# Kernel tuning notes

Hardware: AMD Instinct MI355X
Metric: run time of the kernel (lower is better)

Reference implementation:

```python
import jax, jax.numpy as jnp
import numpy as np

B, D, M, R, C = 4096, 16, 4, 2048, 10
EPS = 1e-9


def setup_inputs() -> dict:
    key = jax.random.key(0)
    k1, k2, k3, k4, k5 = jax.random.split(key, 5)
    x = jax.random.normal(k1, (B, D), dtype=jnp.float32)
    centers = jax.random.normal(k2, (D, M), dtype=jnp.float32)
    widths = jax.random.uniform(k3, (D, M), dtype=jnp.float32, minval=0.5, maxval=1.5)
    consequents = jax.random.uniform(k4, (R, D + 1, C), dtype=jnp.float32)
    rules = jax.random.randint(k5, (R, D), 0, M, dtype=jnp.int32)
    return {"x": x, "centers": centers, "widths": widths,
            "consequents": consequents, "rules": rules}


def reference(x, centers, widths, consequents, rules):
    batch = x.shape[0]
    # Gaussian membership values: (B, D, M)
    mfs = jnp.exp(-((x[:, :, None] - centers[None]) ** 2) / (2.0 * widths[None] ** 2))
    # Gather per-rule memberships: rule_mfs[b, d, r] = mfs[b, d, rules[r, d]] -> (B, D, R)
    idx = jnp.broadcast_to(rules.T[None].astype(jnp.int32), (batch, rules.shape[1], rules.shape[0]))
    rule_mfs = jnp.take_along_axis(mfs, idx, axis=2)
    # Firing strengths: product over input dims -> (B, R)
    fs = jnp.prod(rule_mfs, axis=1)
    norm_fs = fs / (jnp.sum(fs, axis=1, keepdims=True) + EPS)
    # Extended input with bias column -> (B, D+1)
    x_ext = jnp.concatenate([x, jnp.ones((batch, 1), dtype=x.dtype)], axis=1)
    # Faithful to torch.einsum('bi,rjc->brc', ...): i and j are both summed out
    rule_vals = jnp.einsum('bi,rjc->brc', x_ext, consequents)  # (B, R, C)
    out = jnp.einsum('br,brc->bc', norm_fs, rule_vals)  # (B, C)
    return out, norm_fs, x_ext
```

## Files before the change

kernel.cpp:

```cpp
#include <hip/hip_runtime.h>

#define BB 4096
#define DD 16
#define MM 4
#define RR 2048
#define CC 10
#define TB 4
#define RPT (RR / 256)

typedef __attribute__((ext_vector_type(4))) float f32x4;
typedef __attribute__((ext_vector_type(2))) float f32x2;
typedef __attribute__((ext_vector_type(4))) unsigned short u16x4;

__device__ __forceinline__ unsigned short f2bf(float x) {
    union { float f; unsigned u; } v; v.f = x;
    unsigned b = v.u + 0x7FFFu + ((v.u >> 16) & 1u);
    return (unsigned short)(b >> 16);
}
__device__ __forceinline__ float bf2f(unsigned short h) {
    union { unsigned u; float f; } v; v.u = ((unsigned)h) << 16;
    return v.f;
}

__global__ __launch_bounds__(256) void prep_kernel(
    const float* __restrict__ cons, const int* __restrict__ rules,
    float* __restrict__ wsum4a, float* __restrict__ wsum4b,
    float* __restrict__ wsum2, unsigned int* __restrict__ codes)
{
    int gid = blockIdx.x * 256 + threadIdx.x;
    if (gid < RR * CC) {
        int r = gid / CC, c = gid - r * CC;
        const float* cr = cons + (size_t)r * (DD + 1) * CC + c;
        float s = 0.0f;
#pragma unroll
        for (int j = 0; j < DD + 1; ++j) s += cr[j * CC];
        if (c < 4)      wsum4a[r * 4 + c] = s;
        else if (c < 8) wsum4b[r * 4 + (c - 4)] = s;
        else            wsum2[r * 2 + (c - 8)] = s;
    }
    if (gid < RR) {
        const int* rrp = rules + gid * DD;
        unsigned int code = 0;
#pragma unroll
        for (int g = 0; g < 4; ++g) {
            unsigned int byt = 0;
#pragma unroll
            for (int k = 0; k < 4; ++k)
                byt |= (((unsigned int)rrp[g * 4 + k]) & 3u) << (2 * k);
            code |= byt << (8 * g);
        }
        codes[gid] = code;
    }
}

__global__ __launch_bounds__(256, 4) void anfis_main(
    const float* __restrict__ x, const float* __restrict__ centers,
    const float* __restrict__ widths, const f32x4* __restrict__ wsum4a,
    const f32x4* __restrict__ wsum4b, const f32x2* __restrict__ wsum2,
    const unsigned int* __restrict__ codes,
    float* __restrict__ out, float* __restrict__ norm_fs, float* __restrict__ x_ext)
{
    __shared__ __align__(16) char pool[4 * 256 * sizeof(f32x4)];
    f32x4 (*QUAD4)[256] = (f32x4 (*)[256])pool;
    float (*RED)[68]    = (float (*)[68])pool;

    __shared__ u16x4 FS[RR];
    __shared__ float MF[TB][64];
    __shared__ f32x4 PAIR4[8][16];
    __shared__ float xs[TB][DD];
    __shared__ float sx[TB];
    __shared__ float wpart[4][TB];
    __shared__ float invl[TB];
    __shared__ float oscale[TB];
    __shared__ float part2[TB * CC][4];

    const int tid = threadIdx.x;
    const int b0 = blockIdx.x * TB;
    const int lane = tid & 63;
    const int wv = tid >> 6;

    if (tid < TB * (DD + 1)) {
        int row = tid / (DD + 1), col = tid % (DD + 1);
        float v = (col < DD) ? x[(b0 + row) * DD + col] : 1.0f;
        if (col < DD) xs[row][col] = v;
        x_ext[(b0 + row) * (DD + 1) + col] = v;
    }
    __syncthreads();
    if (tid < TB) {
        float s = 1.0f;
#pragma unroll
        for (int d = 0; d < DD; ++d) s += xs[tid][d];
        sx[tid] = s;
    }

    {
        int row = tid >> 6, dm = tid & 63, d = dm >> 2, m = dm & 3;
        float c = centers[d * MM + m];
        float w = widths[d * MM + m];
        float z = xs[row][d] - c;
        MF[row][dm] = expf(-(z * z) / (2.0f * w * w));
    }
    __syncthreads();

    if (tid < 8 * 16) {
        int p = tid >> 4, e = tid & 15;
        int i0 = e & 3, i1 = e >> 2;
        f32x4 v;
#pragma unroll
        for (int row = 0; row < TB; ++row)
            v[row] = MF[row][(2 * p) * 4 + i0] * MF[row][(2 * p + 1) * 4 + i1];
        PAIR4[p][e] = v;
    }
    __syncthreads();

#pragma unroll
    for (int i = tid; i < 4 * 256; i += 256) {
        int g = i >> 8, e = i & 255;
        QUAD4[g][e] = PAIR4[2 * g][e & 15] * PAIR4[2 * g + 1][e >> 4];
    }
    __syncthreads();

    float acc[TB][CC];
#pragma unroll
    for (int row = 0; row < TB; ++row)
#pragma unroll
        for (int c = 0; c < CC; ++c) acc[row][c] = 0.0f;

    f32x4 svec = {0.0f, 0.0f, 0.0f, 0.0f};

#pragma unroll 1
    for (int j = 0; j < RPT; ++j) {
        int r = tid + 256 * j;
        unsigned int code = codes[r];
        f32x4 q0 = QUAD4[0][code & 255u];
        f32x4 q1 = QUAD4[1][(code >> 8) & 255u];
        f32x4 q2 = QUAD4[2][(code >> 16) & 255u];
        f32x4 q3 = QUAD4[3][code >> 24];
        f32x4 p = (q0 * q1) * (q2 * q3);
        svec += p;

        u16x4 fh;
        fh.x = f2bf(p[0]); fh.y = f2bf(p[1]);
        fh.z = f2bf(p[2]); fh.w = f2bf(p[3]);
        FS[r] = fh;

        const f32x4 wa = wsum4a[r];
        const f32x4 wb = wsum4b[r];
        const f32x2 wcp = wsum2[r];
        const float wc[CC] = {wa.x, wa.y, wa.z, wa.w, wb.x,
                              wb.y, wb.z, wb.w, wcp.x, wcp.y};
#pragma unroll
        for (int row = 0; row < TB; ++row)
#pragma unroll
            for (int c = 0; c < CC; ++c)
                acc[row][c] = fmaf(p[row], wc[c], acc[row][c]);
    }

#pragma unroll
    for (int row = 0; row < TB; ++row) {
        float s = svec[row];
#pragma unroll
        for (int off = 32; off > 0; off >>= 1) s += __shfl_xor(s, off, 64);
        if (lane == 0) wpart[wv][row] = s;
    }
    __syncthreads();
    if (tid < TB) {
        float t = wpart[0][tid] + wpart[1][tid] + wpart[2][tid] + wpart[3][tid];
        float inv = 1.0f / (t + 1e-9f);
        invl[tid] = inv;
        oscale[tid] = sx[tid] * inv;
    }
    __syncthreads();

    const float inv0 = invl[0], inv1 = invl[1], inv2 = invl[2], inv3 = invl[3];

#pragma unroll 1
    for (int j = 0; j < RPT; ++j) {
        int r = tid + 256 * j;
        u16x4 fh = FS[r];
        norm_fs[(size_t)(b0 + 0) * RR + r] = bf2f(fh.x) * inv0;
        norm_fs[(size_t)(b0 + 1) * RR + r] = bf2f(fh.y) * inv1;
        norm_fs[(size_t)(b0 + 2) * RR + r] = bf2f(fh.z) * inv2;
        norm_fs[(size_t)(b0 + 3) * RR + r] = bf2f(fh.w) * inv3;
    }

#pragma unroll
    for (int row = 0; row < TB; ++row) {
#pragma unroll
        for (int c = 0; c < CC; ++c) {
            float s = acc[row][c];
            s += __shfl_xor(s, 1, 64);
            s += __shfl_xor(s, 2, 64);
            if ((lane & 3) == 0) RED[row * CC + c][wv * 16 + (lane >> 2)] = s;
        }
    }
    __syncthreads();
    if (tid < 160) {
        int v = tid % 40, ch = tid / 40;
        float s = 0.0f;
        int base = ch * 16;
#pragma unroll
        for (int i = 0; i < 16; ++i) s += RED[v][base + i];
        part2[v][ch] = s;
    }
    __syncthreads();
    if (tid < TB * CC) {
        float val = part2[tid][0] + part2[tid][1] + part2[tid][2] + part2[tid][3];
        int row = tid / CC, c = tid % CC;
        out[(b0 + row) * CC + c] = oscale[row] * val;
    }
}

extern "C" void kernel_launch(void* const* d_in, const int* in_sizes, int n_in,
                              void* d_out, int out_size, void* d_ws, size_t ws_size,
                              hipStream_t stream) {
    const float* x       = (const float*)d_in[0];
    const float* centers = (const float*)d_in[1];
    const float* widths  = (const float*)d_in[2];
    const float* cons    = (const float*)d_in[3];
    const int*   rules   = (const int*)d_in[4];

    float* out_p     = (float*)d_out;
    float* norm_fs_p = out_p + (size_t)BB * CC;
    float* x_ext_p   = norm_fs_p + (size_t)BB * RR;

    float* wsum4a = (float*)d_ws;
    float* wsum4b = wsum4a + (size_t)RR * 4;
    float* wsum2  = wsum4b + (size_t)RR * 4;
    unsigned int* codes = (unsigned int*)(wsum2 + (size_t)RR * 2);

    prep_kernel<<<(RR * CC + 255) / 256, 256, 0, stream>>>(cons, rules, wsum4a,
                                                           wsum4b, wsum2, codes);
    anfis_main<<<BB / TB, 256, 0, stream>>>(x, centers, widths,
                                            (const f32x4*)wsum4a,
                                            (const f32x4*)wsum4b,
                                            (const f32x2*)wsum2, codes,
                                            out_p, norm_fs_p, x_ext_p);
}
```

Measured before the change: 86.74 us.

## Split main kernel into reduction pass and recompute-and-store pass

The fused kernel is split in two. The first kernel computes the firing-strength sums, the per-row inverse normaliser (written to workspace) and the output. The second kernel rebuilds the membership tables, recomputes the firing strengths and writes norm_fs directly. This removes the 16KB bf16 shared buffer and its rounding, which lowers shared memory per block and may raise occupancy. In exchange the table build and product work run twice and there is an extra launch.

```diff
diff --git a/kernel.cpp b/kernel.cpp
--- a/kernel.cpp
+++ b/kernel.cpp
@@ -10,17 +10,6 @@
 
 typedef __attribute__((ext_vector_type(4))) float f32x4;
 typedef __attribute__((ext_vector_type(2))) float f32x2;
-typedef __attribute__((ext_vector_type(4))) unsigned short u16x4;
-
-__device__ __forceinline__ unsigned short f2bf(float x) {
-    union { float f; unsigned u; } v; v.f = x;
-    unsigned b = v.u + 0x7FFFu + ((v.u >> 16) & 1u);
-    return (unsigned short)(b >> 16);
-}
-__device__ __forceinline__ float bf2f(unsigned short h) {
-    union { unsigned u; float f; } v; v.u = ((unsigned)h) << 16;
-    return v.f;
-}
 
 __global__ __launch_bounds__(256) void prep_kernel(
     const float* __restrict__ cons, const int* __restrict__ rules,
@@ -53,24 +42,47 @@
     }
 }
 
-__global__ __launch_bounds__(256, 4) void anfis_main(
+#define BUILD_TABLES(QUADP)  do { \
+    { int row = tid >> 6, dm = tid & 63, d = dm >> 2, m = dm & 3; \
+      float c = centers[d * MM + m]; \
+      float w = widths[d * MM + m]; \
+      float z = xs[row][d] - c; \
+      MF[row][dm] = expf(-(z * z) / (2.0f * w * w)); } \
+    __syncthreads(); \
+    if (tid < 8 * 16) { \
+        int p = tid >> 4, e = tid & 15; \
+        int i0 = e & 3, i1 = e >> 2; \
+        f32x4 v; \
+        _Pragma("unroll") \
+        for (int row = 0; row < TB; ++row) \
+            v[row] = MF[row][(2 * p) * 4 + i0] * MF[row][(2 * p + 1) * 4 + i1]; \
+        PAIR4[p][e] = v; \
+    } \
+    __syncthreads(); \
+    _Pragma("unroll") \
+    for (int i = tid; i < 4 * 256; i += 256) { \
+        int g = i >> 8, e = i & 255; \
+        (QUADP)[g][e] = PAIR4[2 * g][e & 15] * PAIR4[2 * g + 1][e >> 4]; \
+    } \
+    __syncthreads(); \
+} while (0)
+
+__global__ __launch_bounds__(256, 4) void anfis_sum(
     const float* __restrict__ x, const float* __restrict__ centers,
     const float* __restrict__ widths, const f32x4* __restrict__ wsum4a,
     const f32x4* __restrict__ wsum4b, const f32x2* __restrict__ wsum2,
     const unsigned int* __restrict__ codes,
-    float* __restrict__ out, float* __restrict__ norm_fs, float* __restrict__ x_ext)
+    float* __restrict__ out, float* __restrict__ x_ext, float* __restrict__ invg)
 {
     __shared__ __align__(16) char pool[4 * 256 * sizeof(f32x4)];
     f32x4 (*QUAD4)[256] = (f32x4 (*)[256])pool;
     float (*RED)[68]    = (float (*)[68])pool;
 
-    __shared__ u16x4 FS[RR];
     __shared__ float MF[TB][64];
     __shared__ f32x4 PAIR4[8][16];
     __shared__ float xs[TB][DD];
     __shared__ float sx[TB];
     __shared__ float wpart[4][TB];
-    __shared__ float invl[TB];
     __shared__ float oscale[TB];
     __shared__ float part2[TB * CC][4];
 
@@ -93,32 +105,7 @@
         sx[tid] = s;
     }
 
-    {
-        int row = tid >> 6, dm = tid & 63, d = dm >> 2, m = dm & 3;
-        float c = centers[d * MM + m];
-        float w = widths[d * MM + m];
-        float z = xs[row][d] - c;
-        MF[row][dm] = expf(-(z * z) / (2.0f * w * w));
-    }
-    __syncthreads();
-
-    if (tid < 8 * 16) {
-        int p = tid >> 4, e = tid & 15;
-        int i0 = e & 3, i1 = e >> 2;
-        f32x4 v;
-#pragma unroll
-        for (int row = 0; row < TB; ++row)
-            v[row] = MF[row][(2 * p) * 4 + i0] * MF[row][(2 * p + 1) * 4 + i1];
-        PAIR4[p][e] = v;
-    }
-    __syncthreads();
-
-#pragma unroll
-    for (int i = tid; i < 4 * 256; i += 256) {
-        int g = i >> 8, e = i & 255;
-        QUAD4[g][e] = PAIR4[2 * g][e & 15] * PAIR4[2 * g + 1][e >> 4];
-    }
-    __syncthreads();
+    BUILD_TABLES(QUAD4);
 
     float acc[TB][CC];
 #pragma unroll
@@ -139,11 +126,6 @@
         f32x4 p = (q0 * q1) * (q2 * q3);
         svec += p;
 
-        u16x4 fh;
-        fh.x = f2bf(p[0]); fh.y = f2bf(p[1]);
-        fh.z = f2bf(p[2]); fh.w = f2bf(p[3]);
-        FS[r] = fh;
-
         const f32x4 wa = wsum4a[r];
         const f32x4 wb = wsum4b[r];
         const f32x2 wcp = wsum2[r];
@@ -167,23 +149,11 @@
     if (tid < TB) {
         float t = wpart[0][tid] + wpart[1][tid] + wpart[2][tid] + wpart[3][tid];
         float inv = 1.0f / (t + 1e-9f);
-        invl[tid] = inv;
+        invg[b0 + tid] = inv;
         oscale[tid] = sx[tid] * inv;
     }
-    __syncthreads();
-
-    const float inv0 = invl[0], inv1 = invl[1], inv2 = invl[2], inv3 = invl[3];
-
-#pragma unroll 1
-    for (int j = 0; j < RPT; ++j) {
-        int r = tid + 256 * j;
-        u16x4 fh = FS[r];
-        norm_fs[(size_t)(b0 + 0) * RR + r] = bf2f(fh.x) * inv0;
-        norm_fs[(size_t)(b0 + 1) * RR + r] = bf2f(fh.y) * inv1;
-        norm_fs[(size_t)(b0 + 2) * RR + r] = bf2f(fh.z) * inv2;
-        norm_fs[(size_t)(b0 + 3) * RR + r] = bf2f(fh.w) * inv3;
-    }
-
+
+    __syncthreads();
 #pragma unroll
     for (int row = 0; row < TB; ++row) {
 #pragma unroll
@@ -208,6 +178,48 @@
         float val = part2[tid][0] + part2[tid][1] + part2[tid][2] + part2[tid][3];
         int row = tid / CC, c = tid % CC;
         out[(b0 + row) * CC + c] = oscale[row] * val;
+    }
+}
+
+__global__ __launch_bounds__(256, 4) void anfis_store(
+    const float* __restrict__ x, const float* __restrict__ centers,
+    const float* __restrict__ widths, const unsigned int* __restrict__ codes,
+    const float* __restrict__ invg, float* __restrict__ norm_fs)
+{
+    __shared__ __align__(16) f32x4 QUAD4[4][256];
+    __shared__ float MF[TB][64];
+    __shared__ f32x4 PAIR4[8][16];
+    __shared__ float xs[TB][DD];
+
+    const int tid = threadIdx.x;
+    const int b0 = blockIdx.x * TB;
+
+    if (tid < TB * DD) {
+        int row = tid / DD, d = tid % DD;
+        xs[row][d] = x[(b0 + row) * DD + d];
+    }
+    __syncthreads();
+
+    BUILD_TABLES(QUAD4);
+
+    const float inv0 = invg[b0 + 0];
+    const float inv1 = invg[b0 + 1];
+    const float inv2 = invg[b0 + 2];
+    const float inv3 = invg[b0 + 3];
+
+#pragma unroll 1
+    for (int j = 0; j < RPT; ++j) {
+        int r = tid + 256 * j;
+        unsigned int code = codes[r];
+        f32x4 q0 = QUAD4[0][code & 255u];
+        f32x4 q1 = QUAD4[1][(code >> 8) & 255u];
+        f32x4 q2 = QUAD4[2][(code >> 16) & 255u];
+        f32x4 q3 = QUAD4[3][code >> 24];
+        f32x4 p = (q0 * q1) * (q2 * q3);
+        norm_fs[(size_t)(b0 + 0) * RR + r] = p[0] * inv0;
+        norm_fs[(size_t)(b0 + 1) * RR + r] = p[1] * inv1;
+        norm_fs[(size_t)(b0 + 2) * RR + r] = p[2] * inv2;
+        norm_fs[(size_t)(b0 + 3) * RR + r] = p[3] * inv3;
     }
 }
 
@@ -228,12 +240,15 @@
     float* wsum4b = wsum4a + (size_t)RR * 4;
     float* wsum2  = wsum4b + (size_t)RR * 4;
     unsigned int* codes = (unsigned int*)(wsum2 + (size_t)RR * 2);
+    float* invg   = (float*)(codes + RR);
 
     prep_kernel<<<(RR * CC + 255) / 256, 256, 0, stream>>>(cons, rules, wsum4a,
                                                            wsum4b, wsum2, codes);
-    anfis_main<<<BB / TB, 256, 0, stream>>>(x, centers, widths,
-                                            (const f32x4*)wsum4a,
-                                            (const f32x4*)wsum4b,
-                                            (const f32x2*)wsum2, codes,
-                                            out_p, norm_fs_p, x_ext_p);
-}
+    anfis_sum<<<BB / TB, 256, 0, stream>>>(x, centers, widths,
+                                           (const f32x4*)wsum4a,
+                                           (const f32x4*)wsum4b,
+                                           (const f32x2*)wsum2, codes,
+                                           out_p, x_ext_p, invg);
+    anfis_store<<<BB / TB, 256, 0, stream>>>(x, centers, widths, codes,
+                                             invg, norm_fs_p);
+}
```

Measured after the change: 96.80 us. 1.12x slower.
